# Kernel optimization log

Hardware: AMD Instinct MI355X
Metric: run time of the kernel (lower is better)

The kernel has to match this reference:

```python
import jax, jax.numpy as jnp
import numpy as np

VOCAB = 32000
EMBED = 512


def setup_inputs() -> dict:
    key = jax.random.key(0)
    k_idx, k_w, k_b = jax.random.split(key, 3)
    input_indices = jax.random.randint(k_idx, (4, 2048), 0, VOCAB, dtype=jnp.int64)
    # Conv2d(vocab, embed, 1) weight is (embed, vocab, 1, 1); drop trailing 1x1 dims.
    fan_in = VOCAB
    bound = 1.0 / np.sqrt(fan_in)
    W = jax.random.uniform(k_w, (EMBED, VOCAB), jnp.float32, -bound, bound)
    b = jax.random.uniform(k_b, (EMBED,), jnp.float32, -bound, bound)
    return {"input_indices": input_indices, "W": W, "b": b}


def reference(input_indices, W, b):
    # Faithful to the original: one-hot encode then 1x1 conv (a dense GEMM
    # over the vocab axis), which is mathematically W[:, idx] + b.
    B, S = input_indices.shape
    one_hot = jax.nn.one_hot(input_indices, VOCAB, dtype=jnp.float32)  # [B,S,V]
    # 1x1 conv on [N, V, 1, 1] == matmul with W: [B,S,V] x [E,V] -> [B,S,E]
    embedding = jnp.einsum("bsv,ev->bse", one_hot, W) + b
    return embedding
```

## Files before the change

### kernel.cpp

```cpp
#include <hip/hip_runtime.h>
#include <hip/hip_bf16.h>


constexpr int VOCAB  = 32000;
constexpr int EMBED  = 512;
constexpr int VSHIFT = 9;
constexpr int VC     = 1 << VSHIFT;
constexpr int NCHUNK = (VOCAB + VC - 1) / VC;
constexpr int ET     = 16;
constexpr int PAD    = 516;


__global__ __launch_bounds__(1024) void bucket_kernel(
    const int* __restrict__ idx, int* __restrict__ ws, int ntok)
{
    __shared__ int hist[NCHUNK];
    __shared__ int cursor[NCHUNK];
    const int tid = threadIdx.x;

    if (tid < NCHUNK) hist[tid] = 0;
    __syncthreads();

    for (int t = tid; t < ntok; t += 1024)
        atomicAdd(&hist[idx[t] >> VSHIFT], 1);
    __syncthreads();

    if (tid == 0) {
        int run = 0;
        for (int c = 0; c < NCHUNK; ++c) {
            cursor[c]   = run;
            ws[c]       = hist[c];
            ws[64 + c]  = run;
            run += hist[c];
        }
    }
    __syncthreads();

    for (int t = tid; t < ntok; t += 1024) {
        int v = idx[t];
        int c = v >> VSHIFT;
        int p = atomicAdd(&cursor[c], 1);
        ws[128 + p] = (t << VSHIFT) | (v & (VC - 1));
    }
}

__global__ __launch_bounds__(256) void scatter_kernel(
    const float* __restrict__ W,
    const float* __restrict__ bias,
    const int* __restrict__ ws,
    float* __restrict__ out)
{
    __shared__ float chunk[ET][PAD];
    __shared__ float bsh[ET];

    const int cx  = blockIdx.x;
    const int ey  = blockIdx.y;
    const int c0  = cx << VSHIFT;
    const int e0  = ey * ET;
    const int tid = threadIdx.x;

    const int cols = min(VC, VOCAB - c0);
    const int csh  = (cols == VC) ? (VSHIFT - 2) : (VSHIFT - 3);

    for (int i = tid; i < ET * (cols >> 2); i += 256) {
        int r  = i >> csh;
        int c4 = (i & ((1 << csh) - 1)) << 2;
        float4 v = *reinterpret_cast<const float4*>(
            W + (size_t)(e0 + r) * VOCAB + c0 + c4);
        *reinterpret_cast<float4*>(&chunk[0][0] + r * PAD + c4) = v;
    }
    if (tid < ET) bsh[tid] = bias[e0 + tid];

    const int cnt  = ws[cx];
    const int base = ws[64 + cx];
    const int* entries = ws + 128 + base;
    __syncthreads();

    const int total = cnt * ET;
    for (int w = tid; w < total; w += 256) {
        int k  = w >> 4;
        int j  = w & (ET - 1);
        int e  = entries[k];
        int t  = e >> VSHIFT;
        int vl = e & (VC - 1);
        out[(size_t)t * EMBED + e0 + j] = chunk[j][vl] + bsh[j];
    }
}

extern "C" void kernel_launch(void* const* d_in, const int* in_sizes, int n_in,
                              void* d_out, int out_size, void* d_ws, size_t ws_size,
                              hipStream_t stream) {
    const int*   idx  = (const int*)d_in[0];
    const float* W    = (const float*)d_in[1];
    const float* bias = (const float*)d_in[2];
    float* out = (float*)d_out;
    int*   ws  = (int*)d_ws;

    int ntok = in_sizes[0];

    bucket_kernel<<<1, 1024, 0, stream>>>(idx, ws, ntok);

    dim3 grid(NCHUNK, EMBED / ET);
    scatter_kernel<<<grid, 256, 0, stream>>>(W, bias, ws, out);
}
```

Baseline: 111.4 us.

## Use direct global-to-LDS loads, wider embed tiles, and vectorized index bucketing

Result: faster. 107.8 us (-3.3%).

```diff
diff --git a/kernel.cpp b/kernel.cpp
--- a/kernel.cpp
+++ b/kernel.cpp
@@ -7,7 +7,7 @@
 constexpr int VSHIFT = 9;
 constexpr int VC     = 1 << VSHIFT;
 constexpr int NCHUNK = (VOCAB + VC - 1) / VC;
-constexpr int ET     = 16;
+constexpr int ET     = 32;
 constexpr int PAD    = 516;
 
 
@@ -21,36 +21,46 @@
     if (tid < NCHUNK) hist[tid] = 0;
     __syncthreads();
 
-    for (int t = tid; t < ntok; t += 1024)
-        atomicAdd(&hist[idx[t] >> VSHIFT], 1);
+    const int n4 = ntok >> 2;
+    const int4* idx4 = (const int4*)idx;
+    for (int q = tid; q < n4; q += 1024) {
+        int4 v = idx4[q];
+        atomicAdd(&hist[v.x >> VSHIFT], 1);
+        atomicAdd(&hist[v.y >> VSHIFT], 1);
+        atomicAdd(&hist[v.z >> VSHIFT], 1);
+        atomicAdd(&hist[v.w >> VSHIFT], 1);
+    }
     __syncthreads();
 
     if (tid == 0) {
         int run = 0;
         for (int c = 0; c < NCHUNK; ++c) {
-            cursor[c]   = run;
-            ws[c]       = hist[c];
-            ws[64 + c]  = run;
+            cursor[c]  = run;
+            ws[c]      = hist[c];
+            ws[64 + c] = run;
             run += hist[c];
         }
     }
     __syncthreads();
 
-    for (int t = tid; t < ntok; t += 1024) {
-        int v = idx[t];
-        int c = v >> VSHIFT;
-        int p = atomicAdd(&cursor[c], 1);
-        ws[128 + p] = (t << VSHIFT) | (v & (VC - 1));
+    for (int q = tid; q < n4; q += 1024) {
+        int4 v = idx4[q];
+        int t = q << 2;
+        int p;
+        p = atomicAdd(&cursor[v.x >> VSHIFT], 1); ws[128 + p] = ((t + 0) << VSHIFT) | (v.x & (VC - 1));
+        p = atomicAdd(&cursor[v.y >> VSHIFT], 1); ws[128 + p] = ((t + 1) << VSHIFT) | (v.y & (VC - 1));
+        p = atomicAdd(&cursor[v.z >> VSHIFT], 1); ws[128 + p] = ((t + 2) << VSHIFT) | (v.z & (VC - 1));
+        p = atomicAdd(&cursor[v.w >> VSHIFT], 1); ws[128 + p] = ((t + 3) << VSHIFT) | (v.w & (VC - 1));
     }
 }
 
-__global__ __launch_bounds__(256) void scatter_kernel(
+__global__ __launch_bounds__(512) void scatter_kernel(
     const float* __restrict__ W,
     const float* __restrict__ bias,
     const int* __restrict__ ws,
     float* __restrict__ out)
 {
-    __shared__ float chunk[ET][PAD];
+    __shared__ float chunk[ET * PAD];
     __shared__ float bsh[ET];
 
     const int cx  = blockIdx.x;
@@ -60,14 +70,19 @@
     const int tid = threadIdx.x;
 
     const int cols = min(VC, VOCAB - c0);
-    const int csh  = (cols == VC) ? (VSHIFT - 2) : (VSHIFT - 3);
+    const int cpr  = cols >> 8;
+    const int nck  = ET * cpr;
 
-    for (int i = tid; i < ET * (cols >> 2); i += 256) {
-        int r  = i >> csh;
-        int c4 = (i & ((1 << csh) - 1)) << 2;
-        float4 v = *reinterpret_cast<const float4*>(
-            W + (size_t)(e0 + r) * VOCAB + c0 + c4);
-        *reinterpret_cast<float4*>(&chunk[0][0] + r * PAD + c4) = v;
+    const int wv   = tid >> 6;
+    const int lane = tid & 63;
+    for (int c = wv; c < nck; c += 8) {
+        int r = (cpr == 2) ? (c >> 1) : c;
+        int h = (cpr == 2) ? (c & 1) : 0;
+        const float* src = W + (size_t)(e0 + r) * VOCAB + c0 + (h << 8) + (lane << 2);
+        float* dst = &chunk[r * PAD + (h << 8)];
+        __builtin_amdgcn_global_load_lds(
+            (const __attribute__((address_space(1))) void*)src,
+            (__attribute__((address_space(3))) void*)dst, 16, 0, 0);
     }
     if (tid < ET) bsh[tid] = bias[e0 + tid];
 
@@ -76,14 +91,15 @@
     const int* entries = ws + 128 + base;
     __syncthreads();
 
-    const int total = cnt * ET;
-    for (int w = tid; w < total; w += 256) {
-        int k  = w >> 4;
-        int j  = w & (ET - 1);
+    const int j    = tid & 31;
+    const int rowb = j * PAD;
+    const float bv = bsh[j];
+    for (int k = tid >> 5; k < cnt; k += 16) {
         int e  = entries[k];
         int t  = e >> VSHIFT;
         int vl = e & (VC - 1);
-        out[(size_t)t * EMBED + e0 + j] = chunk[j][vl] + bsh[j];
+        float val = chunk[rowb + vl] + bv;
+        __builtin_nontemporal_store(val, &out[(size_t)t * EMBED + e0 + j]);
     }
 }
 
@@ -101,5 +117,5 @@
     bucket_kernel<<<1, 1024, 0, stream>>>(idx, ws, ntok);
 
     dim3 grid(NCHUNK, EMBED / ET);
-    scatter_kernel<<<grid, 256, 0, stream>>>(W, bias, ws, out);
+    scatter_kernel<<<grid, 512, 0, stream>>>(W, bias, ws, out);
 }
```
